# Optimization experiments

Measured on AMD Instinct MI355X. Metric: run time of the kernel, lower is better.

The kernel has to match this reference:

```python
import jax, jax.numpy as jnp
import numpy as np

M_MARGIN = 0.25
GAMMA = 64.0
EPS = 1e-5


def _circle_loss_one_way(enc, dec):
    # enc, dec: [N, D]. Faithful to the torch rotate-concat construction:
    # cos_sim[j, k] = cosine(enc[j], dec[(j + k) % N]); column 0 is the positive.
    N = enc.shape[0]
    dot = enc @ dec.T                                   # [N, N]
    en = jnp.sqrt(jnp.sum(enc * enc, axis=1, keepdims=True))   # [N, 1]
    dn = jnp.sqrt(jnp.sum(dec * dec, axis=1, keepdims=True))   # [N, 1]
    S = dot / (en * dn.T + EPS)                         # [N, N] cosine sims
    r = jnp.arange(N)
    idx = (r[:, None] + r[None, :]) % N                 # [N, N] rolled column index
    cos_sim = jnp.take_along_axis(S, idx, axis=1)       # [N, N]
    sp = cos_sim[:, 0:1]                                # [N, 1] positives (diag of S)
    sn = cos_sim[:, 1:]                                 # [N, N-1] negatives
    ap = jnp.maximum(-jax.lax.stop_gradient(sp) + 1.0 + M_MARGIN, 0.0)
    an = jnp.maximum(jax.lax.stop_gradient(sn) + M_MARGIN, 0.0)
    delta_p = 1.0 - M_MARGIN
    delta_n = M_MARGIN
    logit_p = -ap * (sp - delta_p) * GAMMA              # [N, 1]
    logit_n = an * (sn - delta_n) * GAMMA               # [N, N-1]
    lse_n = jax.nn.logsumexp(logit_n, axis=0)           # [N-1]
    lse_p = jax.nn.logsumexp(logit_p, axis=0)           # [1] (cols of repeated sp are identical)
    return jax.nn.softplus(lse_n + lse_p)               # [N-1]


def reference(encoder_output, decoder_output):
    loss_a = _circle_loss_one_way(encoder_output, decoder_output)
    loss_b = _circle_loss_one_way(decoder_output, encoder_output)
    return jnp.mean((loss_a + loss_b) / 2.0)


def setup_inputs() -> dict:
    key = jax.random.key(0)
    k1, k2 = jax.random.split(key)
    N, D = 8192, 128
    return {
        "encoder_output": jax.random.normal(k1, (N, D), dtype=jnp.float32),
        "decoder_output": jax.random.normal(k2, (N, D), dtype=jnp.float32),
    }
```

## Files before the change

kernel.cpp:

```cpp
#include <hip/hip_runtime.h>
#include <hip/hip_bf16.h>

#define NN 8192

using bf16x8 = __attribute__((ext_vector_type(8))) short;
using f32x4  = __attribute__((ext_vector_type(4))) float;

#if __has_builtin(__builtin_amdgcn_exp2f)
#define EXP2(x) __builtin_amdgcn_exp2f(x)
#else
#define EXP2(x) __expf((x) * 0.69314718056f)
#endif

__device__ __forceinline__ void gl_lds16(const void* g, void* l) {
  __builtin_amdgcn_global_load_lds(
      (const __attribute__((address_space(1))) unsigned int*)(unsigned long long)g,
      (__attribute__((address_space(3))) unsigned int*)(unsigned int)(unsigned long long)l,
      16, 0, 0);
}

__global__ __launch_bounds__(256) void k_prep(const float* __restrict__ enc,
                                              const float* __restrict__ dec,
                                              unsigned* __restrict__ Abf,
                                              unsigned* __restrict__ Bbf,
                                              float* __restrict__ logit_p,
                                              float* __restrict__ bandsum,
                                              unsigned* __restrict__ counter) {
  const int t = threadIdx.x;
  const int l16 = t & 15;
  const int row = blockIdx.x * 16 + (t >> 4);
  const int tid = blockIdx.x * 256 + t;
  if (tid < 64 * 256) bandsum[tid] = 0.0f;
  if (tid == 64 * 256) *counter = 0u;

  const float4* e4 = reinterpret_cast<const float4*>(enc) + (size_t)row * 32 + l16 * 2;
  const float4* d4 = reinterpret_cast<const float4*>(dec) + (size_t)row * 32 + l16 * 2;
  float4 e0 = e4[0], e1 = e4[1];
  float4 d0 = d4[0], d1 = d4[1];

  float se = e0.x*e0.x + e0.y*e0.y + e0.z*e0.z + e0.w*e0.w
           + e1.x*e1.x + e1.y*e1.y + e1.z*e1.z + e1.w*e1.w;
  float sd = d0.x*d0.x + d0.y*d0.y + d0.z*d0.z + d0.w*d0.w
           + d1.x*d1.x + d1.y*d1.y + d1.z*d1.z + d1.w*d1.w;
  float sp = e0.x*d0.x + e0.y*d0.y + e0.z*d0.z + e0.w*d0.w
           + e1.x*d1.x + e1.y*d1.y + e1.z*d1.z + e1.w*d1.w;
#pragma unroll
  for (int off = 1; off < 16; off <<= 1) {
    se += __shfl_xor(se, off);
    sd += __shfl_xor(sd, off);
    sp += __shfl_xor(sp, off);
  }
  float ie = rsqrtf(se), id = rsqrtf(sd);

  union { __hip_bfloat162 h; unsigned u; } p;
  uint4 ua, ub;
  p.h = __float22bfloat162_rn(make_float2(e0.x * ie, e0.y * ie)); ua.x = p.u;
  p.h = __float22bfloat162_rn(make_float2(e0.z * ie, e0.w * ie)); ua.y = p.u;
  p.h = __float22bfloat162_rn(make_float2(e1.x * ie, e1.y * ie)); ua.z = p.u;
  p.h = __float22bfloat162_rn(make_float2(e1.z * ie, e1.w * ie)); ua.w = p.u;
  p.h = __float22bfloat162_rn(make_float2(d0.x * id, d0.y * id)); ub.x = p.u;
  p.h = __float22bfloat162_rn(make_float2(d0.z * id, d0.w * id)); ub.y = p.u;
  p.h = __float22bfloat162_rn(make_float2(d1.x * id, d1.y * id)); ub.z = p.u;
  p.h = __float22bfloat162_rn(make_float2(d1.z * id, d1.w * id)); ub.w = p.u;
  reinterpret_cast<uint4*>(Abf)[(size_t)row * 16 + l16] = ua;
  reinterpret_cast<uint4*>(Bbf)[(size_t)row * 16 + l16] = ub;

  if (l16 == 0) {
    float en = se * ie, dn = sd * id;
    float s  = sp / (en * dn + 1e-5f);
    logit_p[row] = -fmaxf(1.25f - s, 0.0f) * (s - 0.75f) * 64.0f;
  }
}

__global__ __launch_bounds__(256, 2) void k_main(const unsigned short* __restrict__ A,
                                                 const unsigned short* __restrict__ B,
                                                 float* __restrict__ bandsum,
                                                 const float* __restrict__ logit_p,
                                                 unsigned* __restrict__ counter,
                                                 float* __restrict__ out) {
  __shared__ __align__(16) unsigned short As[128 * 128];
  __shared__ __align__(16) unsigned short Bs[128 * 128];
  __shared__ float part[4][256];
  __shared__ unsigned lastFlag;

  const int t  = threadIdx.x;
  const int T  = blockIdx.x;
  const int sp = blockIdx.y;

#pragma unroll
  for (int q = 0; q < 4; ++q) part[q][t] = 0.0f;

  const int lane = t & 63;
  const int w = t >> 6, wrow = w >> 1, wcol = w & 1;
  const int l15 = lane & 15, quad = lane >> 4;
  const int x7 = l15 & 7;

  const unsigned short* Abase = As + (wrow * 64 + l15) * 128;
  const unsigned short* Bbase = Bs + (wcol * 64 + l15) * 128;
  char* AsB = (char*)As;
  char* BsB = (char*)Bs;

  float dreg[28];
#pragma unroll
  for (int i = 0; i < 28; ++i) dreg[i] = 0.0f;

  const int rl_lo = t >> 4;
  const int lgoff = rl_lo * 256 + ((t & 15) ^ (rl_lo & 7)) * 16;
  const int lloff = t * 16;

  {
    const int by = sp * 8;
    const int bx = (by + T) & 63;
    const char* AgT = (const char*)A + (size_t)by * 32768 + lgoff;
    const char* BgT = (const char*)B + (size_t)bx * 32768 + lgoff;
#pragma unroll
    for (int j = 0; j < 8; ++j) {
      gl_lds16(AgT + j * 4096, AsB + lloff + j * 4096);
      gl_lds16(BgT + j * 4096, BsB + lloff + j * 4096);
    }
  }
  __syncthreads();

  for (int it = 0; it < 8; ++it) {
    f32x4 acc[4][4];
    const f32x4 zv = {0.f, 0.f, 0.f, 0.f};
#pragma unroll
    for (int r = 0; r < 4; ++r)
#pragma unroll
      for (int c = 0; c < 4; ++c) acc[r][c] = zv;

#pragma unroll
    for (int ks = 0; ks < 4; ++ks) {
      bf16x8 a[4], b[4];
      const int off = ((ks * 4 + quad) ^ x7) * 8;
#pragma unroll
      for (int r = 0; r < 4; ++r)
        a[r] = *reinterpret_cast<const bf16x8*>(Abase + r * 16 * 128 + off);
#pragma unroll
      for (int c = 0; c < 4; ++c)
        b[c] = *reinterpret_cast<const bf16x8*>(Bbase + c * 16 * 128 + off);
#pragma unroll
      for (int r = 0; r < 4; ++r)
#pragma unroll
        for (int c = 0; c < 4; ++c)
          acc[r][c] = __builtin_amdgcn_mfma_f32_16x16x32_bf16(a[r], b[c], acc[r][c], 0, 0, 0);
    }

    __syncthreads();

    if (it < 7) {
      const int by = sp * 8 + it + 1;
      const int bx = (by + T) & 63;
      const char* AgT = (const char*)A + (size_t)by * 32768 + lgoff;
      const char* BgT = (const char*)B + (size_t)bx * 32768 + lgoff;
#pragma unroll
      for (int j = 0; j < 8; ++j) {
        gl_lds16(AgT + j * 4096, AsB + lloff + j * 4096);
        gl_lds16(BgT + j * 4096, BsB + lloff + j * 4096);
      }
    }

#pragma unroll
    for (int dlt = -3; dlt <= 3; ++dlt) {
#pragma unroll
      for (int g = 0; g < 4; ++g) {
        float s = 0.0f;
#pragma unroll
        for (int r = 0; r < 4; ++r) {
          int c = r + dlt;
          if (c < 0 || c > 3) continue;
          float sn = acc[r][c][g];
          float an = fmaxf(sn + 0.25f, 0.0f);
          float u  = fmaf(sn, 92.332483f, -23.083121f);
          s += EXP2(an * u);
        }
        dreg[(dlt + 3) * 4 + g] += s;
      }
    }

    __syncthreads();
  }

  const int  Qoff = (wcol - wrow) * 64 + 127;
  const int  v    = l15 - quad * 4;
  const bool leader = (quad == 0) || (l15 <= 3);
  const bool ok1 = (l15 <= 11) && (quad <= 2);
  const bool ok2 = (l15 <= 7)  && (quad <= 1);

#pragma unroll
  for (int dlt = -3; dlt <= 3; ++dlt) {
#pragma unroll
    for (int g = 0; g < 4; ++g) {
      float s = dreg[(dlt + 3) * 4 + g];
      float t1 = __shfl_down(s, 20); s += ok1 ? t1 : 0.0f;
      float t2 = __shfl_down(s, 40); s += ok2 ? t2 : 0.0f;
      int ld = Qoff + dlt * 16 - g + v;
      if (leader) unsafeAtomicAdd(&part[w][ld], s);
    }
  }
  __syncthreads();

  if (t < 255) {
    float vv = part[0][t] + part[1][t] + part[2][t] + part[3][t];
    unsafeAtomicAdd(&bandsum[T * 256 + t], vv);
  }

  __syncthreads();
  if (t == 0) lastFlag = (atomicAdd(counter, 1u) == 511u) ? 1u : 0u;
  __syncthreads();
  if (!lastFlag) return;

  __threadfence();
  float* sm = part[0];

  float lp[32];
#pragma unroll
  for (int k = 0; k < 32; ++k) lp[k] = logit_p[t + 256 * k];

  float m = lp[0];
#pragma unroll
  for (int k = 1; k < 32; ++k) m = fmaxf(m, lp[k]);
#pragma unroll
  for (int off = 32; off; off >>= 1) m = fmaxf(m, __shfl_down(m, off));
  if (lane == 0) sm[w] = m;
  __syncthreads();
  m = fmaxf(fmaxf(sm[0], sm[1]), fmaxf(sm[2], sm[3]));
  __syncthreads();

  float s = 0.0f;
#pragma unroll
  for (int k = 0; k < 32; ++k) s += __expf(lp[k] - m);
#pragma unroll
  for (int off = 32; off; off >>= 1) s += __shfl_down(s, off);
  if (lane == 0) sm[w] = s;
  __syncthreads();
  s = sm[0] + sm[1] + sm[2] + sm[3];
  float lse_p = m + __logf(s);
  __syncthreads();

  const int o  = t & 127;
  const int hi = t >> 7;
  float bs1[32], bs2[32];
#pragma unroll
  for (int k = 0; k < 32; ++k) {
    int Ta = hi + 2 * k;
    bs1[k] = bandsum[Ta * 256 + o + 127];
    bs2[k] = o ? bandsum[((Ta + 1) & 63) * 256 + o - 1] : 0.0f;
  }
  float acc = 0.0f;
#pragma unroll
  for (int k = 0; k < 32; ++k) {
    if (t == 0 && k == 0) continue;
    float se = bs1[k] + bs2[k];
    float x = __logf(se) + lse_p;
    acc += fmaxf(x, 0.0f) + __logf(1.0f + __expf(-fabsf(x)));
  }
#pragma unroll
  for (int off = 32; off; off >>= 1) acc += __shfl_down(acc, off);
  if (lane == 0) sm[w] = acc;
  __syncthreads();
  if (t == 0) out[0] = (sm[0] + sm[1] + sm[2] + sm[3]) * (1.0f / 8191.0f);
}

extern "C" void kernel_launch(void* const* d_in, const int* in_sizes, int n_in,
                              void* d_out, int out_size, void* d_ws, size_t ws_size,
                              hipStream_t stream) {
  const float* enc = (const float*)d_in[0];
  const float* dec = (const float*)d_in[1];
  float* ws = (float*)d_ws;

  float*    logit_p = ws;
  float*    bandsum = ws + 8192;
  unsigned* counter = (unsigned*)(ws + 8192 + 16384);
  unsigned* Abf     = (unsigned*)(ws + 8192 + 16384 + 256);
  unsigned* Bbf     = Abf + 524288;
  float*    out     = (float*)d_out;

  k_prep<<<NN / 16, 256, 0, stream>>>(enc, dec, Abf, Bbf, logit_p, bandsum, counter);
  dim3 grid(64, 8);
  k_main<<<grid, 256, 0, stream>>>((const unsigned short*)Abf, (const unsigned short*)Bbf,
                                   bandsum, logit_p, counter, out);
}
```

Baseline: 102.7 us.

## Switch similarity GEMM to FP8 MFMA with double-buffered LDS tiles

The prep kernel now quantizes the normalized encoder/decoder rows to FP8 (e4m3) instead of bf16. The main kernel uses the 16x16x32 fp8 MFMA, which halves global and LDS traffic per tile. It also double-buffers the LDS tiles so the next tile's global->LDS loads are issued before the current tile's MFMAs. The gain is less data movement and better overlap of loads with compute. The risk is accuracy: FP8 cosine similarities feed exponentials scaled by gamma=64, so quantization error is amplified in the loss.

```diff
diff --git a/kernel.cpp b/kernel.cpp
--- a/kernel.cpp
+++ b/kernel.cpp
@@ -3,8 +3,7 @@
 
 #define NN 8192
 
-using bf16x8 = __attribute__((ext_vector_type(8))) short;
-using f32x4  = __attribute__((ext_vector_type(4))) float;
+using f32x4 = __attribute__((ext_vector_type(4))) float;
 
 #if __has_builtin(__builtin_amdgcn_exp2f)
 #define EXP2(x) __builtin_amdgcn_exp2f(x)
@@ -19,10 +18,41 @@
       16, 0, 0);
 }
 
+#if __has_builtin(__builtin_amdgcn_cvt_pk_fp8_f32)
+__device__ __forceinline__ unsigned pk4_fp8(float x0, float x1, float x2, float x3) {
+  unsigned w = (unsigned)__builtin_amdgcn_cvt_pk_fp8_f32(x0, x1, 0, false);
+  w = (unsigned)__builtin_amdgcn_cvt_pk_fp8_f32(x2, x3, (int)w, true);
+  return w;
+}
+#else
+__device__ __forceinline__ unsigned f8_1(float f) {
+  unsigned u = __float_as_uint(f);
+  unsigned s = (u >> 24) & 0x80u;
+  float a = fabsf(f);
+  if (a < 0.015625f) {
+    unsigned m = (unsigned)rintf(a * 512.0f);
+    return s | (m > 7u ? 8u : m);
+  }
+  if (a > 448.0f) return s | 0x7Eu;
+  unsigned au = u & 0x7FFFFFFFu;
+  unsigned e = (au >> 23) - 127u + 7u;
+  unsigned m23 = au & 0x7FFFFFu;
+  unsigned m = m23 >> 20;
+  unsigned rem = m23 & 0xFFFFFu;
+  if (rem > 0x80000u || (rem == 0x80000u && (m & 1u))) {
+    if (++m == 8u) { m = 0u; ++e; }
+  }
+  return s | (e << 3) | m;
+}
+__device__ __forceinline__ unsigned pk4_fp8(float x0, float x1, float x2, float x3) {
+  return f8_1(x0) | (f8_1(x1) << 8) | (f8_1(x2) << 16) | (f8_1(x3) << 24);
+}
+#endif
+
 __global__ __launch_bounds__(256) void k_prep(const float* __restrict__ enc,
                                               const float* __restrict__ dec,
-                                              unsigned* __restrict__ Abf,
-                                              unsigned* __restrict__ Bbf,
+                                              uint2* __restrict__ A8,
+                                              uint2* __restrict__ B8,
                                               float* __restrict__ logit_p,
                                               float* __restrict__ bandsum,
                                               unsigned* __restrict__ counter) {
@@ -52,18 +82,13 @@
   }
   float ie = rsqrtf(se), id = rsqrtf(sd);
 
-  union { __hip_bfloat162 h; unsigned u; } p;
-  uint4 ua, ub;
-  p.h = __float22bfloat162_rn(make_float2(e0.x * ie, e0.y * ie)); ua.x = p.u;
-  p.h = __float22bfloat162_rn(make_float2(e0.z * ie, e0.w * ie)); ua.y = p.u;
-  p.h = __float22bfloat162_rn(make_float2(e1.x * ie, e1.y * ie)); ua.z = p.u;
-  p.h = __float22bfloat162_rn(make_float2(e1.z * ie, e1.w * ie)); ua.w = p.u;
-  p.h = __float22bfloat162_rn(make_float2(d0.x * id, d0.y * id)); ub.x = p.u;
-  p.h = __float22bfloat162_rn(make_float2(d0.z * id, d0.w * id)); ub.y = p.u;
-  p.h = __float22bfloat162_rn(make_float2(d1.x * id, d1.y * id)); ub.z = p.u;
-  p.h = __float22bfloat162_rn(make_float2(d1.z * id, d1.w * id)); ub.w = p.u;
-  reinterpret_cast<uint4*>(Abf)[(size_t)row * 16 + l16] = ua;
-  reinterpret_cast<uint4*>(Bbf)[(size_t)row * 16 + l16] = ub;
+  uint2 ua, ub;
+  ua.x = pk4_fp8(e0.x * ie, e0.y * ie, e0.z * ie, e0.w * ie);
+  ua.y = pk4_fp8(e1.x * ie, e1.y * ie, e1.z * ie, e1.w * ie);
+  ub.x = pk4_fp8(d0.x * id, d0.y * id, d0.z * id, d0.w * id);
+  ub.y = pk4_fp8(d1.x * id, d1.y * id, d1.z * id, d1.w * id);
+  A8[(size_t)row * 16 + l16] = ua;
+  B8[(size_t)row * 16 + l16] = ub;
 
   if (l16 == 0) {
     float en = se * ie, dn = sd * id;
@@ -72,14 +97,14 @@
   }
 }
 
-__global__ __launch_bounds__(256, 2) void k_main(const unsigned short* __restrict__ A,
-                                                 const unsigned short* __restrict__ B,
+__global__ __launch_bounds__(256, 2) void k_main(const unsigned char* __restrict__ A,
+                                                 const unsigned char* __restrict__ B,
                                                  float* __restrict__ bandsum,
                                                  const float* __restrict__ logit_p,
                                                  unsigned* __restrict__ counter,
                                                  float* __restrict__ out) {
-  __shared__ __align__(16) unsigned short As[128 * 128];
-  __shared__ __align__(16) unsigned short Bs[128 * 128];
+  __shared__ __align__(16) unsigned char As[2 * 16384];
+  __shared__ __align__(16) unsigned char Bs[2 * 16384];
   __shared__ float part[4][256];
   __shared__ unsigned lastFlag;
 
@@ -94,70 +119,77 @@
   const int w = t >> 6, wrow = w >> 1, wcol = w & 1;
   const int l15 = lane & 15, quad = lane >> 4;
   const int x7 = l15 & 7;
-
-  const unsigned short* Abase = As + (wrow * 64 + l15) * 128;
-  const unsigned short* Bbase = Bs + (wcol * 64 + l15) * 128;
-  char* AsB = (char*)As;
-  char* BsB = (char*)Bs;
+  const int qh = quad >> 1, ql8 = (quad & 1) * 8;
+
+  const int rl = t >> 3;
+  const int lgoff = rl * 128 + ((t & 7) ^ (rl & 7)) * 16;
+  const int lloff = t * 16;
+
+  const char* Ab = (const char*)A;
+  const char* Bb = (const char*)B;
 
   float dreg[28];
 #pragma unroll
   for (int i = 0; i < 28; ++i) dreg[i] = 0.0f;
 
-  const int rl_lo = t >> 4;
-  const int lgoff = rl_lo * 256 + ((t & 15) ^ (rl_lo & 7)) * 16;
-  const int lloff = t * 16;
+  const int arow = (wrow * 64 + l15) * 128;
+  const int brow = (wcol * 64 + l15) * 128;
 
   {
     const int by = sp * 8;
     const int bx = (by + T) & 63;
-    const char* AgT = (const char*)A + (size_t)by * 32768 + lgoff;
-    const char* BgT = (const char*)B + (size_t)bx * 32768 + lgoff;
-#pragma unroll
-    for (int j = 0; j < 8; ++j) {
-      gl_lds16(AgT + j * 4096, AsB + lloff + j * 4096);
-      gl_lds16(BgT + j * 4096, BsB + lloff + j * 4096);
+    const char* Ag = Ab + (size_t)by * 16384 + lgoff;
+    const char* Bg = Bb + (size_t)bx * 16384 + lgoff;
+#pragma unroll
+    for (int j = 0; j < 4; ++j) {
+      gl_lds16(Ag + j * 4096, (char*)As + j * 4096 + lloff);
+      gl_lds16(Bg + j * 4096, (char*)Bs + j * 4096 + lloff);
     }
   }
   __syncthreads();
 
   for (int it = 0; it < 8; ++it) {
-    f32x4 acc[4][4];
-    const f32x4 zv = {0.f, 0.f, 0.f, 0.f};
-#pragma unroll
-    for (int r = 0; r < 4; ++r)
-#pragma unroll
-      for (int c = 0; c < 4; ++c) acc[r][c] = zv;
-
-#pragma unroll
-    for (int ks = 0; ks < 4; ++ks) {
-      bf16x8 a[4], b[4];
-      const int off = ((ks * 4 + quad) ^ x7) * 8;
-#pragma unroll
-      for (int r = 0; r < 4; ++r)
-        a[r] = *reinterpret_cast<const bf16x8*>(Abase + r * 16 * 128 + off);
-#pragma unroll
-      for (int c = 0; c < 4; ++c)
-        b[c] = *reinterpret_cast<const bf16x8*>(Bbase + c * 16 * 128 + off);
-#pragma unroll
-      for (int r = 0; r < 4; ++r)
-#pragma unroll
-        for (int c = 0; c < 4; ++c)
-          acc[r][c] = __builtin_amdgcn_mfma_f32_16x16x32_bf16(a[r], b[c], acc[r][c], 0, 0, 0);
-    }
-
-    __syncthreads();
+    const int p = it & 1;
 
     if (it < 7) {
       const int by = sp * 8 + it + 1;
       const int bx = (by + T) & 63;
-      const char* AgT = (const char*)A + (size_t)by * 32768 + lgoff;
-      const char* BgT = (const char*)B + (size_t)bx * 32768 + lgoff;
-#pragma unroll
-      for (int j = 0; j < 8; ++j) {
-        gl_lds16(AgT + j * 4096, AsB + lloff + j * 4096);
-        gl_lds16(BgT + j * 4096, BsB + lloff + j * 4096);
+      const char* Ag = Ab + (size_t)by * 16384 + lgoff;
+      const char* Bg = Bb + (size_t)bx * 16384 + lgoff;
+      char* Ad = (char*)As + (p ^ 1) * 16384 + lloff;
+      char* Bd = (char*)Bs + (p ^ 1) * 16384 + lloff;
+#pragma unroll
+      for (int j = 0; j < 4; ++j) {
+        gl_lds16(Ag + j * 4096, Ad + j * 4096);
+        gl_lds16(Bg + j * 4096, Bd + j * 4096);
       }
+    }
+
+    f32x4 acc[4][4];
+    const f32x4 zv = {0.f, 0.f, 0.f, 0.f};
+#pragma unroll
+    for (int r = 0; r < 4; ++r)
+#pragma unroll
+      for (int c = 0; c < 4; ++c) acc[r][c] = zv;
+
+    const char* Abuf = (const char*)As + p * 16384;
+    const char* Bbuf = (const char*)Bs + p * 16384;
+
+#pragma unroll
+    for (int ks = 0; ks < 4; ++ks) {
+      long a[4], b[4];
+      const int off = (((ks * 2 + qh) ^ x7) * 16) + ql8;
+#pragma unroll
+      for (int r = 0; r < 4; ++r)
+        a[r] = *reinterpret_cast<const long*>(Abuf + arow + r * 2048 + off);
+#pragma unroll
+      for (int c = 0; c < 4; ++c)
+        b[c] = *reinterpret_cast<const long*>(Bbuf + brow + c * 2048 + off);
+#pragma unroll
+      for (int r = 0; r < 4; ++r)
+#pragma unroll
+        for (int c = 0; c < 4; ++c)
+          acc[r][c] = __builtin_amdgcn_mfma_f32_16x16x32_fp8_fp8(a[r], b[c], acc[r][c], 0, 0, 0);
     }
 
 #pragma unroll
@@ -272,12 +304,12 @@
   float*    logit_p = ws;
   float*    bandsum = ws + 8192;
   unsigned* counter = (unsigned*)(ws + 8192 + 16384);
-  unsigned* Abf     = (unsigned*)(ws + 8192 + 16384 + 256);
-  unsigned* Bbf     = Abf + 524288;
+  uint2*    A8      = (uint2*)(ws + 8192 + 16384 + 256);
+  uint2*    B8      = (uint2*)((char*)A8 + 1048576);
   float*    out     = (float*)d_out;
 
-  k_prep<<<NN / 16, 256, 0, stream>>>(enc, dec, Abf, Bbf, logit_p, bandsum, counter);
+  k_prep<<<NN / 16, 256, 0, stream>>>(enc, dec, A8, B8, logit_p, bandsum, counter);
   dim3 grid(64, 8);
-  k_main<<<grid, 256, 0, stream>>>((const unsigned short*)Abf, (const unsigned short*)Bbf,
+  k_main<<<grid, 256, 0, stream>>>((const unsigned char*)A8, (const unsigned char*)B8,
                                    bandsum, logit_p, counter, out);
 }
```

After: 96.38 us. 1.07x faster.
